# Kernel optimization log

Hardware: AMD Instinct MI355X
Metric: run time of the kernel (lower is better)

The kernel has to match this reference:

```python
import jax, jax.numpy as jnp
import numpy as np

N = 2708
IN_C = 1433
OUT_C = 64


def setup_inputs() -> dict:
    key = jax.random.key(0)
    k1, k2, k3, k4, k5, k6, k7 = jax.random.split(key, 7)
    X = jax.random.normal(k1, (N, IN_C), dtype=jnp.float32)
    A = jax.random.randint(k2, (N, N), 0, 2, dtype=jnp.int32)  # dense binary adjacency mask
    # Graph Fourier basis: orthonormal-ish random matrix (QR of gaussian)
    U = jnp.linalg.qr(jax.random.normal(k3, (N, N), dtype=jnp.float32))[0]
    s = 1.0 / np.sqrt(IN_C)
    W_K = jax.random.normal(k4, (OUT_C, IN_C), dtype=jnp.float32) * s
    W_Q = jax.random.normal(k5, (OUT_C, IN_C), dtype=jnp.float32) * s
    W_V = jax.random.normal(k6, (OUT_C, IN_C), dtype=jnp.float32) * s
    lmbd = jax.random.uniform(k7, (N, 1), dtype=jnp.float32)
    return {"X": X, "A": A, "U": U, "W_K": W_K, "W_Q": W_Q, "W_V": W_V, "lmbd": lmbd}


def reference(X, A, U, W_K, W_Q, W_V, lmbd):
    # Linear projections (torch nn.Linear: x @ W.T)
    K = X @ W_K.T  # [N, d]
    Q = X @ W_Q.T  # [N, d]
    V = X @ W_V.T  # [N, d]
    d_k = K.shape[-1]
    E = (Q @ K.T) / d_k  # [N, N]
    # spectral filtering: igft(lmbd * gft(E)) = U @ (lmbd * (U^T @ E))
    E = jnp.abs(U @ (lmbd * (U.T @ E)))
    # masked softmax over neighbors; dropout p=0 in eval mode (no-op)
    E_masked = jnp.where(A == 0, -jnp.inf, E)
    alpha = jax.nn.softmax(E_masked, axis=-1)
    H = alpha @ V  # [N, d]
    return H
```

## Files before the change

### kernel.cpp

```cpp
#include <hip/hip_runtime.h>

#define NV 2708
#define INC 1433
#define XCOLS 1472
#define UDIM 2752
#define PSTR 2728
#define BSTR 2752
#define SLAB ((size_t)(2752*64))
#define MWPR 88
#define NSP 8
#define NSU 11

typedef __attribute__((ext_vector_type(8))) short bf16x8;
typedef __attribute__((ext_vector_type(4))) float f32x4;
typedef __attribute__((ext_vector_type(4))) unsigned short u16x4;

__device__ __forceinline__ unsigned short f2bf(float f){
  union { float f; unsigned int i; } v; v.f = f;
  return (unsigned short)((v.i + 0x7fffu + ((v.i >> 16) & 1u)) >> 16);
}

__device__ __forceinline__ void conv_row(const float* __restrict__ src,
                                         unsigned short* __restrict__ dst, int tid){
  const int sh = ((unsigned int)((size_t)src >> 2)) & 1;
  if (tid == 0){ int ce = sh ? 0 : (INC - 1); dst[ce] = f2bf(src[ce]); }
  const float2* s2 = (const float2*)(src + sh);
  for (int c2 = tid; c2 < (INC - 1)/2; c2 += 256){
    float2 v = s2[c2];
    int c = sh + c2*2;
    dst[c]     = f2bf(v.x);
    dst[c + 1] = f2bf(v.y);
  }
  for (int c = INC + tid; c < XCOLS; c += 256) dst[c] = 0;
}

__global__ __launch_bounds__(256) void convert_all(
    const float* __restrict__ X, const float* __restrict__ WK,
    const float* __restrict__ WQ, const float* __restrict__ WV,
    const float* __restrict__ U, const int* __restrict__ A,
    unsigned short* __restrict__ Xbf, unsigned short* __restrict__ Wbf,
    unsigned short* __restrict__ Ubf, unsigned short* __restrict__ UTbf,
    unsigned int* __restrict__ Abits)
{
  __shared__ __align__(16) float tpose[64][68];
  const int bx = blockIdx.x;
  const int tid = threadIdx.x;
  if (bx < 2752){
    const int row = bx;
    unsigned short* dst = Ubf + (size_t)row*UDIM;
    if (row < NV){
      const float* src = U + (size_t)row*NV;
      for (int c4 = tid; c4 < 688; c4 += 256){
        float4 v = make_float4(0.f,0.f,0.f,0.f);
        if (c4 < 677) v = *(const float4*)(src + c4*4);
        u16x4 h = { f2bf(v.x), f2bf(v.y), f2bf(v.z), f2bf(v.w) };
        *(u16x4*)(dst + c4*4) = h;
      }
    } else {
      u16x4 zz = {0,0,0,0};
      for (int c4 = tid; c4 < 688; c4 += 256) *(u16x4*)(dst + c4*4) = zz;
    }
  } else if (bx < 5504){
    const int row = bx - 2752;
    unsigned short* dst = Xbf + (size_t)row*XCOLS;
    if (row < NV){
      conv_row(X + (size_t)row*INC, dst, tid);
    } else {
      u16x4 zz = {0,0,0,0};
      for (int c4 = tid; c4 < XCOLS/4; c4 += 256) *(u16x4*)(dst + c4*4) = zz;
    }
  } else if (bx < 5696){
    const int row = bx - 5504;
    const float* s = (row < 64) ? WK : (row < 128) ? WQ : WV;
    conv_row(s + (size_t)(row & 63)*INC, Wbf + (size_t)row*XCOLS, tid);
  } else if (bx < 8404){
    const int i = bx - 5696;
    const int lane = tid & 63, wave = tid >> 6;
    const int* arow = A + (size_t)i*NV;
    unsigned int* drow = Abits + (size_t)i*MWPR;
    for (int g = wave; g < 11; g += 4){
      int base = g*256 + lane*4;
      int4 v = make_int4(0,0,0,0);
      if (base < NV) v = *(const int4*)(arow + base);
      unsigned long long m0 = __ballot(v.x != 0);
      unsigned long long m1 = __ballot(v.y != 0);
      unsigned long long m2 = __ballot(v.z != 0);
      unsigned long long m3 = __ballot(v.w != 0);
      if (lane < 8){
        unsigned long long mm = (lane < 2) ? m0 : (lane < 4) ? m1 : (lane < 6) ? m2 : m3;
        drow[g*8 + lane] = (lane & 1) ? (unsigned int)(mm >> 32) : (unsigned int)mm;
      }
    }
  } else {
    const int t = bx - 8404;
    const int tx = t % 43, ty = t / 43;
    const int r0 = ty*64, c0 = tx*64;
    #pragma unroll
    for (int j = 0; j < 4; j++){
      int row = j*16 + (tid >> 4);
      int c4  = (tid & 15)*4;
      float4 v = make_float4(0.f,0.f,0.f,0.f);
      if (r0 + row < NV && c0 + c4 < NV)
        v = *(const float4*)(U + (size_t)(r0+row)*NV + c0 + c4);
      *(float4*)&tpose[row][c4] = v;
    }
    __syncthreads();
    const int i = tid >> 2;
    #pragma unroll
    for (int j = 0; j < 4; j++){
      int kk = ((tid & 3) + j*4)*4;
      u16x4 h = { f2bf(tpose[kk+0][i]), f2bf(tpose[kk+1][i]),
                  f2bf(tpose[kk+2][i]), f2bf(tpose[kk+3][i]) };
      *(u16x4*)(UTbf + (size_t)(c0+i)*UDIM + r0 + kk) = h;
    }
  }
}

__global__ __launch_bounds__(256) void proj(
    const unsigned short* __restrict__ Xbf, const unsigned short* __restrict__ Wbf,
    float* __restrict__ part)
{
  __shared__ __align__(16) unsigned short At[64*72];
  __shared__ __align__(16) unsigned short Bt[64*72];
  const int tid = threadIdx.x;
  const int lane = tid & 63, wave = tid >> 6, quad = lane >> 4, lr = lane & 15;
  const int m0 = blockIdx.x * 64;
  const int s  = blockIdx.y, z = blockIdx.z;
  const int kbeg = s * 192, kend = min(kbeg + 192, XCOLS);
  const int wm = (wave & 1) * 32, wn = (wave >> 1) * 32;
  const unsigned short* Wz = Wbf + (size_t)z*64*XCOLS;
  const int srow = wave*8 + (lane >> 3), seg = lane & 7;
  f32x4 acc[2][2] = {};

  for (int k0 = kbeg; k0 < kend; k0 += 64){
    #pragma unroll
    for (int e = 0; e < 2; e++){
      int row = e*32 + srow;
      bf16x8 xa = *(const bf16x8*)(Xbf + (size_t)(m0+row)*XCOLS + k0 + seg*8);
      bf16x8 wb = *(const bf16x8*)(Wz  + (size_t)row*XCOLS      + k0 + seg*8);
      *(bf16x8*)&At[row*72 + seg*8] = xa;
      *(bf16x8*)&Bt[row*72 + seg*8] = wb;
    }
    __syncthreads();
    #pragma unroll
    for (int ks = 0; ks < 2; ks++){
      bf16x8 af[2], bv[2];
      #pragma unroll
      for (int t = 0; t < 2; t++){
        af[t] = *(const bf16x8*)&At[(wm + t*16 + lr)*72 + ks*32 + quad*8];
        bv[t] = *(const bf16x8*)&Bt[(wn + t*16 + lr)*72 + ks*32 + quad*8];
      }
      #pragma unroll
      for (int tm = 0; tm < 2; tm++)
        #pragma unroll
        for (int tn = 0; tn < 2; tn++)
          acc[tm][tn] = __builtin_amdgcn_mfma_f32_16x16x32_bf16(af[tm], bv[tn], acc[tm][tn], 0, 0, 0);
    }
    __syncthreads();
  }
  float* dst = part + (size_t)(z*NSP + s) * SLAB;
  #pragma unroll
  for (int tm = 0; tm < 2; tm++)
    #pragma unroll
    for (int tn = 0; tn < 2; tn++)
      #pragma unroll
      for (int e = 0; e < 4; e++)
        dst[(size_t)(m0 + wm + tm*16 + quad*4 + e)*64 + wn + tn*16 + lr] = acc[tm][tn][e];
}

__global__ __launch_bounds__(256) void reduce_proj(
    const float* __restrict__ part, unsigned short* __restrict__ K16f,
    unsigned short* __restrict__ QT16, unsigned short* __restrict__ VTf)
{
  int idx = blockIdx.x*256 + threadIdx.x;
  int z = blockIdx.y;
  int m = idx >> 6, c = idx & 63;
  const float* base = part + (size_t)z*NSP*SLAB + idx;
  float v = 0.f;
  #pragma unroll
  for (int s = 0; s < NSP; s++) v += base[s*SLAB];
  unsigned short h = (m < NV) ? f2bf(v) : (unsigned short)0;
  if (z == 0){
    if (m < 2720) K16f[((m>>4)*2 + (c>>5))*512 + (m&15)*32 + (c&31)] = h;
  } else if (z == 1){
    QT16[(size_t)c*BSTR + m] = h;
  } else {
    if (m < 2720) VTf[(m>>5)*2048 + c*32 + (m&31)] = h;
  }
}

__global__ __launch_bounds__(256) void gemmU(
    const unsigned short* __restrict__ Arow, const unsigned short* __restrict__ Bcm,
    float* __restrict__ part)
{
  __shared__ __align__(16) unsigned short At[32*72];
  __shared__ __align__(16) unsigned short Bt[64*72];
  const int tid = threadIdx.x;
  const int lane = tid & 63, wave = tid >> 6, quad = lane >> 4, lr = lane & 15;
  const int m0 = blockIdx.x * 32;
  const int s  = blockIdx.y;
  const int kbeg = s * 256, kend = min(kbeg + 256, UDIM);
  const int wm = (wave & 1) * 16, wn = (wave >> 1) * 32;
  const int arow = tid >> 3, aseg = tid & 7;
  const int bc = tid >> 2, bseg = tid & 3;
  f32x4 acc[2] = {};

  for (int k0 = kbeg; k0 < kend; k0 += 64){
    *(bf16x8*)&At[arow*72 + aseg*8] =
        *(const bf16x8*)(Arow + (size_t)(m0+arow)*UDIM + k0 + aseg*8);
    {
      const unsigned short* b = Bcm + (size_t)bc*BSTR + k0 + bseg*16;
      *(bf16x8*)&Bt[bc*72 + bseg*16]     = *(const bf16x8*)(b);
      *(bf16x8*)&Bt[bc*72 + bseg*16 + 8] = *(const bf16x8*)(b + 8);
    }
    __syncthreads();
    #pragma unroll
    for (int ks = 0; ks < 2; ks++){
      bf16x8 af = *(const bf16x8*)&At[(wm + lr)*72 + ks*32 + quad*8];
      bf16x8 bv[2];
      #pragma unroll
      for (int t = 0; t < 2; t++)
        bv[t] = *(const bf16x8*)&Bt[(wn + t*16 + lr)*72 + ks*32 + quad*8];
      #pragma unroll
      for (int t = 0; t < 2; t++)
        acc[t] = __builtin_amdgcn_mfma_f32_16x16x32_bf16(af, bv[t], acc[t], 0, 0, 0);
    }
    __syncthreads();
  }
  float* dst = part + (size_t)s * SLAB;
  #pragma unroll
  for (int t = 0; t < 2; t++)
    #pragma unroll
    for (int e = 0; e < 4; e++)
      dst[(size_t)(m0 + wm + quad*4 + e)*64 + wn + t*16 + lr] = acc[t][e];
}

__global__ __launch_bounds__(256) void reduce_g(
    const float* __restrict__ part, const float* __restrict__ lm,
    unsigned short* __restrict__ G2T)
{
  int idx = blockIdx.x*256 + threadIdx.x;
  int m = idx >> 6, c = idx & 63;
  const float* base = part + idx;
  float v = 0.f;
  #pragma unroll
  for (int s = 0; s < NSU; s++) v += base[s*SLAB];
  unsigned short h = 0;
  if (m < NV) h = f2bf(v * lm[m] * (1.0f/64.0f));
  G2T[(size_t)c*BSTR + m] = h;
}

__global__ __launch_bounds__(512) void fused_attn(
    const float* __restrict__ partF, const unsigned short* __restrict__ K16f,
    const unsigned int* __restrict__ Abits, const unsigned short* __restrict__ VTf,
    float* __restrict__ Hout)
{
  __shared__ __align__(16) unsigned short pbuf[16*PSTR];
  __shared__ __align__(16) unsigned short fbuf[16*64];
  __shared__ unsigned int mrow[16*MWPR];
  __shared__ float swave[8][16];
  __shared__ float rinv[16];
  __shared__ __align__(16) float obuf[4][256];
  const int tid  = threadIdx.x;
  const int lane = tid & 63, wave = tid >> 6;
  const int quad = lane >> 4, lr = lane & 15;
  const int i0 = blockIdx.x * 16;

  #pragma unroll
  for (int h = 0; h < 2; h++){
    int idx = h*512 + tid;
    const float* base = partF + (size_t)(i0 + (idx >> 6))*64 + (idx & 63);
    float v = 0.f;
    #pragma unroll
    for (int s = 0; s < NSU; s++) v += base[s*SLAB];
    fbuf[idx] = f2bf(v);
  }
  for (int idx = tid; idx < 16*MWPR; idx += 512){
    int r = idx / MWPR;
    unsigned int v = 0;
    if (i0 + r < NV) v = Abits[(size_t)(i0 + r)*MWPR + (idx - r*MWPR)];
    mrow[idx] = v;
  }
  __syncthreads();

  const bf16x8 af0 = *(const bf16x8*)&fbuf[lr*64 + quad*8];
  const bf16x8 af1 = *(const bf16x8*)&fbuf[lr*64 + 32 + quad*8];
  float psum[4] = {0.f, 0.f, 0.f, 0.f};
  {
    int t = wave;
    const unsigned short* kb = K16f + t*1024 + lr*32 + quad*8;
    bf16x8 b0 = *(const bf16x8*)(kb);
    bf16x8 b1 = *(const bf16x8*)(kb + 512);
    while (t < 170){
      int tn = t + 8;
      bf16x8 n0 = b0, n1 = b1;
      if (tn < 170){
        const unsigned short* nb = K16f + tn*1024 + lr*32 + quad*8;
        n0 = *(const bf16x8*)(nb);
        n1 = *(const bf16x8*)(nb + 512);
      }
      f32x4 sv0 = {}, sv1 = {};
      sv0 = __builtin_amdgcn_mfma_f32_16x16x32_bf16(af0, b0, sv0, 0, 0, 0);
      sv1 = __builtin_amdgcn_mfma_f32_16x16x32_bf16(af1, b1, sv1, 0, 0, 0);
      f32x4 sv = sv0 + sv1;
      {
        int col = t*16 + lr;
        int ss = col & 255, ll = ss >> 2;
        int wsh = (col >> 8)*8 + (ss & 3)*2 + (ll >> 5);
        int bit = ll & 31;
        #pragma unroll
        for (int e = 0; e < 4; e++){
          int r = quad*4 + e;
          float p = 0.f;
          if ((mrow[r*MWPR + wsh] >> bit) & 1u) p = __expf(fabsf(sv[e]));
          psum[e] += p;
          pbuf[r*PSTR + col] = f2bf(p);
        }
      }
      b0 = n0; b1 = n1; t = tn;
    }
  }
  #pragma unroll
  for (int e = 0; e < 4; e++){
    float v = psum[e];
    #pragma unroll
    for (int o = 1; o <= 8; o <<= 1) v += __shfl_xor(v, o, 64);
    if (lr == 0) swave[wave][quad*4 + e] = v;
  }
  __syncthreads();
  if (tid < 16){
    float s = 0.f;
    #pragma unroll
    for (int w = 0; w < 8; w++) s += swave[w][tid];
    rinv[tid] = (s > 0.f) ? (1.f/s) : 0.f;
  }
  __syncthreads();

  const int c0 = (wave & 3) * 16;
  const int ktbeg = (wave >> 2) ? 43 : 0;
  const int ktend = (wave >> 2) ? 85 : 43;
  f32x4 acc = {};
  {
    bf16x8 bv = *(const bf16x8*)&VTf[ktbeg*2048 + (c0 + lr)*32 + quad*8];
    for (int kt = ktbeg; kt < ktend; kt++){
      bf16x8 bn = bv;
      if (kt + 1 < ktend) bn = *(const bf16x8*)&VTf[(kt+1)*2048 + (c0 + lr)*32 + quad*8];
      bf16x8 af = *(const bf16x8*)&pbuf[lr*PSTR + kt*32 + quad*8];
      acc = __builtin_amdgcn_mfma_f32_16x16x32_bf16(af, bv, acc, 0, 0, 0);
      bv = bn;
    }
  }
  if (wave >= 4) *(f32x4*)&obuf[wave & 3][lane*4] = acc;
  __syncthreads();
  if (wave < 4){
    f32x4 o = *(const f32x4*)&obuf[wave][lane*4];
    acc += o;
    #pragma unroll
    for (int e = 0; e < 4; e++){
      int r = quad*4 + e;
      int i = i0 + r;
      if (i < NV) Hout[(size_t)i*64 + c0 + lr] = acc[e] * rinv[r];
    }
  }
}

extern "C" void kernel_launch(void* const* d_in, const int* in_sizes, int n_in,
                              void* d_out, int out_size, void* d_ws, size_t ws_size,
                              hipStream_t stream){
  (void)in_sizes; (void)n_in; (void)out_size; (void)ws_size;
  const float* X  = (const float*)d_in[0];
  const int*   A  = (const int*)d_in[1];
  const float* U  = (const float*)d_in[2];
  const float* WK = (const float*)d_in[3];
  const float* WQ = (const float*)d_in[4];
  const float* WV = (const float*)d_in[5];
  const float* lm = (const float*)d_in[6];

  char* ws = (char*)d_ws;
  size_t off = 0;
  auto alloc = [&](size_t bytes){ size_t o = off; off = (off + bytes + 255) & ~(size_t)255; return o; };
  float*          part = (float*)(ws + alloc(24*SLAB*4));
  unsigned short* Ubf  = (unsigned short*)(ws + alloc((size_t)UDIM*UDIM*2));
  unsigned short* UTbf = (unsigned short*)(ws + alloc((size_t)UDIM*UDIM*2));
  unsigned short* Xbf  = (unsigned short*)(ws + alloc((size_t)UDIM*XCOLS*2));
  unsigned short* Wbf  = (unsigned short*)(ws + alloc((size_t)192*XCOLS*2));
  unsigned short* K16f = (unsigned short*)(ws + alloc((size_t)170*1024*2));
  unsigned short* QT16 = (unsigned short*)(ws + alloc((size_t)64*BSTR*2));
  unsigned short* G2T  = (unsigned short*)(ws + alloc((size_t)64*BSTR*2));
  unsigned short* VTf  = (unsigned short*)(ws + alloc((size_t)85*2048*2));
  unsigned int*   Abits= (unsigned int*)(ws + alloc((size_t)NV*MWPR*4));

  convert_all<<<dim3(10253), 256, 0, stream>>>(X, WK, WQ, WV, U, A,
                                               Xbf, Wbf, Ubf, UTbf, Abits);
  proj<<<dim3(43, NSP, 3), 256, 0, stream>>>(Xbf, Wbf, part);
  reduce_proj<<<dim3(688, 3), 256, 0, stream>>>(part, K16f, QT16, VTf);
  gemmU<<<dim3(86, NSU), 256, 0, stream>>>(UTbf, QT16, part);
  reduce_g<<<dim3(688), 256, 0, stream>>>(part, lm, G2T);
  gemmU<<<dim3(86, NSU), 256, 0, stream>>>(Ubf, G2T, part);
  fused_attn<<<dim3(170), 512, 0, stream>>>(part, K16f, Abits, VTf, (float*)d_out);
}
```

Baseline: 177.0 us.

## Fuse U bf16 conversion into transpose tiles and drop LDS staging in GEMMs

Converts U to bf16 inside the same 64x64 tile pass that builds U-transpose, so U is read from global memory once instead of twice and the separate row-conversion blocks disappear. The projection and gemmU kernels no longer stage tiles through shared memory with barriers. Each wave now loads MFMA fragments directly from global memory. The projection uses 32-row tiles with fewer K splits. This removes LDS traffic and synchronisation but adds redundant global/L2 reads across waves and gives less latency hiding per load.

```diff
diff --git a/kernel.cpp b/kernel.cpp
--- a/kernel.cpp
+++ b/kernel.cpp
@@ -8,7 +8,7 @@
 #define BSTR 2752
 #define SLAB ((size_t)(2752*64))
 #define MWPR 88
-#define NSP 8
+#define NSP 4
 #define NSU 11
 
 typedef __attribute__((ext_vector_type(8))) short bf16x8;
@@ -47,21 +47,6 @@
   const int tid = threadIdx.x;
   if (bx < 2752){
     const int row = bx;
-    unsigned short* dst = Ubf + (size_t)row*UDIM;
-    if (row < NV){
-      const float* src = U + (size_t)row*NV;
-      for (int c4 = tid; c4 < 688; c4 += 256){
-        float4 v = make_float4(0.f,0.f,0.f,0.f);
-        if (c4 < 677) v = *(const float4*)(src + c4*4);
-        u16x4 h = { f2bf(v.x), f2bf(v.y), f2bf(v.z), f2bf(v.w) };
-        *(u16x4*)(dst + c4*4) = h;
-      }
-    } else {
-      u16x4 zz = {0,0,0,0};
-      for (int c4 = tid; c4 < 688; c4 += 256) *(u16x4*)(dst + c4*4) = zz;
-    }
-  } else if (bx < 5504){
-    const int row = bx - 2752;
     unsigned short* dst = Xbf + (size_t)row*XCOLS;
     if (row < NV){
       conv_row(X + (size_t)row*INC, dst, tid);
@@ -69,12 +54,12 @@
       u16x4 zz = {0,0,0,0};
       for (int c4 = tid; c4 < XCOLS/4; c4 += 256) *(u16x4*)(dst + c4*4) = zz;
     }
-  } else if (bx < 5696){
-    const int row = bx - 5504;
+  } else if (bx < 2944){
+    const int row = bx - 2752;
     const float* s = (row < 64) ? WK : (row < 128) ? WQ : WV;
     conv_row(s + (size_t)(row & 63)*INC, Wbf + (size_t)row*XCOLS, tid);
-  } else if (bx < 8404){
-    const int i = bx - 5696;
+  } else if (bx < 5652){
+    const int i = bx - 2944;
     const int lane = tid & 63, wave = tid >> 6;
     const int* arow = A + (size_t)i*NV;
     unsigned int* drow = Abits + (size_t)i*MWPR;
@@ -92,7 +77,7 @@
       }
     }
   } else {
-    const int t = bx - 8404;
+    const int t = bx - 5652;
     const int tx = t % 43, ty = t / 43;
     const int r0 = ty*64, c0 = tx*64;
     #pragma unroll
@@ -103,6 +88,8 @@
       if (r0 + row < NV && c0 + c4 < NV)
         v = *(const float4*)(U + (size_t)(r0+row)*NV + c0 + c4);
       *(float4*)&tpose[row][c4] = v;
+      u16x4 h = { f2bf(v.x), f2bf(v.y), f2bf(v.z), f2bf(v.w) };
+      *(u16x4*)(Ubf + (size_t)(r0+row)*UDIM + c0 + c4) = h;
     }
     __syncthreads();
     const int i = tid >> 2;
@@ -120,52 +107,30 @@
     const unsigned short* __restrict__ Xbf, const unsigned short* __restrict__ Wbf,
     float* __restrict__ part)
 {
-  __shared__ __align__(16) unsigned short At[64*72];
-  __shared__ __align__(16) unsigned short Bt[64*72];
   const int tid = threadIdx.x;
   const int lane = tid & 63, wave = tid >> 6, quad = lane >> 4, lr = lane & 15;
-  const int m0 = blockIdx.x * 64;
+  const int m0 = blockIdx.x * 32;
   const int s  = blockIdx.y, z = blockIdx.z;
-  const int kbeg = s * 192, kend = min(kbeg + 192, XCOLS);
-  const int wm = (wave & 1) * 32, wn = (wave >> 1) * 32;
-  const unsigned short* Wz = Wbf + (size_t)z*64*XCOLS;
-  const int srow = wave*8 + (lane >> 3), seg = lane & 7;
-  f32x4 acc[2][2] = {};
-
-  for (int k0 = kbeg; k0 < kend; k0 += 64){
-    #pragma unroll
-    for (int e = 0; e < 2; e++){
-      int row = e*32 + srow;
-      bf16x8 xa = *(const bf16x8*)(Xbf + (size_t)(m0+row)*XCOLS + k0 + seg*8);
-      bf16x8 wb = *(const bf16x8*)(Wz  + (size_t)row*XCOLS      + k0 + seg*8);
-      *(bf16x8*)&At[row*72 + seg*8] = xa;
-      *(bf16x8*)&Bt[row*72 + seg*8] = wb;
-    }
-    __syncthreads();
-    #pragma unroll
-    for (int ks = 0; ks < 2; ks++){
-      bf16x8 af[2], bv[2];
-      #pragma unroll
-      for (int t = 0; t < 2; t++){
-        af[t] = *(const bf16x8*)&At[(wm + t*16 + lr)*72 + ks*32 + quad*8];
-        bv[t] = *(const bf16x8*)&Bt[(wn + t*16 + lr)*72 + ks*32 + quad*8];
-      }
-      #pragma unroll
-      for (int tm = 0; tm < 2; tm++)
-        #pragma unroll
-        for (int tn = 0; tn < 2; tn++)
-          acc[tm][tn] = __builtin_amdgcn_mfma_f32_16x16x32_bf16(af[tm], bv[tn], acc[tm][tn], 0, 0, 0);
-    }
-    __syncthreads();
+  const int kbeg = s * 384, kend = min(kbeg + 384, XCOLS);
+  const int wm = (wave & 1) * 16, wn = (wave >> 1) * 32;
+  const unsigned short* xr = Xbf + (size_t)(m0 + wm + lr)*XCOLS + quad*8;
+  const unsigned short* w0 = Wbf + (size_t)(z*64 + wn + lr)*XCOLS + quad*8;
+  const unsigned short* w1 = Wbf + (size_t)(z*64 + wn + 16 + lr)*XCOLS + quad*8;
+  f32x4 acc[2] = {};
+
+  for (int k0 = kbeg; k0 < kend; k0 += 32){
+    bf16x8 af = *(const bf16x8*)(xr + k0);
+    bf16x8 b0 = *(const bf16x8*)(w0 + k0);
+    bf16x8 b1 = *(const bf16x8*)(w1 + k0);
+    acc[0] = __builtin_amdgcn_mfma_f32_16x16x32_bf16(af, b0, acc[0], 0, 0, 0);
+    acc[1] = __builtin_amdgcn_mfma_f32_16x16x32_bf16(af, b1, acc[1], 0, 0, 0);
   }
   float* dst = part + (size_t)(z*NSP + s) * SLAB;
   #pragma unroll
-  for (int tm = 0; tm < 2; tm++)
-    #pragma unroll
-    for (int tn = 0; tn < 2; tn++)
-      #pragma unroll
-      for (int e = 0; e < 4; e++)
-        dst[(size_t)(m0 + wm + tm*16 + quad*4 + e)*64 + wn + tn*16 + lr] = acc[tm][tn][e];
+  for (int t = 0; t < 2; t++)
+    #pragma unroll
+    for (int e = 0; e < 4; e++)
+      dst[(size_t)(m0 + wm + quad*4 + e)*64 + wn + t*16 + lr] = acc[t][e];
 }
 
 __global__ __launch_bounds__(256) void reduce_proj(
@@ -193,39 +158,23 @@
     const unsigned short* __restrict__ Arow, const unsigned short* __restrict__ Bcm,
     float* __restrict__ part)
 {
-  __shared__ __align__(16) unsigned short At[32*72];
-  __shared__ __align__(16) unsigned short Bt[64*72];
   const int tid = threadIdx.x;
   const int lane = tid & 63, wave = tid >> 6, quad = lane >> 4, lr = lane & 15;
   const int m0 = blockIdx.x * 32;
   const int s  = blockIdx.y;
   const int kbeg = s * 256, kend = min(kbeg + 256, UDIM);
   const int wm = (wave & 1) * 16, wn = (wave >> 1) * 32;
-  const int arow = tid >> 3, aseg = tid & 7;
-  const int bc = tid >> 2, bseg = tid & 3;
+  const unsigned short* ar = Arow + (size_t)(m0 + wm + lr)*UDIM + quad*8;
+  const unsigned short* b0r = Bcm + (size_t)(wn + lr)*BSTR + quad*8;
+  const unsigned short* b1r = Bcm + (size_t)(wn + 16 + lr)*BSTR + quad*8;
   f32x4 acc[2] = {};
 
-  for (int k0 = kbeg; k0 < kend; k0 += 64){
-    *(bf16x8*)&At[arow*72 + aseg*8] =
-        *(const bf16x8*)(Arow + (size_t)(m0+arow)*UDIM + k0 + aseg*8);
-    {
-      const unsigned short* b = Bcm + (size_t)bc*BSTR + k0 + bseg*16;
-      *(bf16x8*)&Bt[bc*72 + bseg*16]     = *(const bf16x8*)(b);
-      *(bf16x8*)&Bt[bc*72 + bseg*16 + 8] = *(const bf16x8*)(b + 8);
-    }
-    __syncthreads();
-    #pragma unroll
-    for (int ks = 0; ks < 2; ks++){
-      bf16x8 af = *(const bf16x8*)&At[(wm + lr)*72 + ks*32 + quad*8];
-      bf16x8 bv[2];
-      #pragma unroll
-      for (int t = 0; t < 2; t++)
-        bv[t] = *(const bf16x8*)&Bt[(wn + t*16 + lr)*72 + ks*32 + quad*8];
-      #pragma unroll
-      for (int t = 0; t < 2; t++)
-        acc[t] = __builtin_amdgcn_mfma_f32_16x16x32_bf16(af, bv[t], acc[t], 0, 0, 0);
-    }
-    __syncthreads();
+  for (int k0 = kbeg; k0 < kend; k0 += 32){
+    bf16x8 af = *(const bf16x8*)(ar + k0);
+    bf16x8 b0 = *(const bf16x8*)(b0r + k0);
+    bf16x8 b1 = *(const bf16x8*)(b1r + k0);
+    acc[0] = __builtin_amdgcn_mfma_f32_16x16x32_bf16(af, b0, acc[0], 0, 0, 0);
+    acc[1] = __builtin_amdgcn_mfma_f32_16x16x32_bf16(af, b1, acc[1], 0, 0, 0);
   }
   float* dst = part + (size_t)s * SLAB;
   #pragma unroll
@@ -390,9 +339,9 @@
   unsigned short* VTf  = (unsigned short*)(ws + alloc((size_t)85*2048*2));
   unsigned int*   Abits= (unsigned int*)(ws + alloc((size_t)NV*MWPR*4));
 
-  convert_all<<<dim3(10253), 256, 0, stream>>>(X, WK, WQ, WV, U, A,
-                                               Xbf, Wbf, Ubf, UTbf, Abits);
-  proj<<<dim3(43, NSP, 3), 256, 0, stream>>>(Xbf, Wbf, part);
+  convert_all<<<dim3(7501), 256, 0, stream>>>(X, WK, WQ, WV, U, A,
+                                              Xbf, Wbf, Ubf, UTbf, Abits);
+  proj<<<dim3(86, NSP, 3), 256, 0, stream>>>(Xbf, Wbf, part);
   reduce_proj<<<dim3(688, 3), 256, 0, stream>>>(part, K16f, QT16, VTf);
   gemmU<<<dim3(86, NSU), 256, 0, stream>>>(UTbf, QT16, part);
   reduce_g<<<dim3(688), 256, 0, stream>>>(part, lm, G2T);
```

Result: slower. 205.4 us (+16.0%).
